# Performance work log

Hardware: AMD Instinct MI355X
Metric: run time of the kernel (lower is better)

## Reference

```python
import jax, jax.numpy as jnp
import numpy as np

ETA = 0.5  # from init_kwargs; eta >= 0 branch
N = 16777216

def setup_inputs() -> dict:
    key = jax.random.key(0)
    k1, k2 = jax.random.split(key)
    outputs = jax.random.normal(k1, (N,), dtype=jnp.float32)
    # PNU targets in {-1, 0, 1}
    targets = jax.random.randint(k2, (N,), 0, 3, dtype=jnp.int32) - 1
    p_ratio = jnp.array([0.4, 0.6], dtype=jnp.float32)
    return {"outputs": outputs, "targets": targets, "p_ratio": p_ratio}

def reference(outputs, targets, p_ratio):
    y = outputs.reshape(-1)
    t = targets.reshape(-1).astype(y.dtype)

    # masks (computed once, fused)
    idx_p = jnp.maximum(t, 0.0)          # positive examples
    idx_n = jnp.maximum(-t, 0.0)         # negative examples
    idx_u = 1.0 - jnp.abs(t)             # unlabeled examples

    sig_neg = jax.nn.sigmoid(-y)         # loss_func(-y)
    sig_pos = jax.nn.sigmoid(y)          # loss_func(-(-y))

    n_p = jnp.maximum(1.0, jnp.sum(idx_p))
    n_n = jnp.maximum(1.0, jnp.sum(idx_n))
    n_u = jnp.maximum(1.0, jnp.sum(idx_u))

    R_P_plus  = jnp.sum(idx_p * sig_neg) / n_p
    R_P_minus = jnp.sum(idx_p * sig_pos) / n_p
    R_N_minus = jnp.sum(idx_n * sig_pos) / n_n
    R_U_minus = jnp.sum(idx_u * sig_pos) / n_u

    R_PN = p_ratio[0] * R_P_plus + p_ratio[1] * R_N_minus
    R_PU = p_ratio[0] * (R_P_plus - R_P_minus) + R_U_minus

    # eta >= 0 branch
    return (1.0 - ETA) * R_PN + ETA * R_PU
```

## Files before the change

kernel.cpp:

```cpp
#include <hip/hip_runtime.h>

#define ETA 0.5f
#define NTHREADS 256
#define UNROLL 4
#define CHUNK (NTHREADS * UNROLL)
#define NCHUNKS 4
#define NACC 5

__device__ __forceinline__ float wave_reduce_sum(float v) {
#pragma unroll
    for (int off = 32; off > 0; off >>= 1)
        v += __shfl_down(v, off, 64);
    return v;
}

__device__ __forceinline__ void pnu_accum(float yy, int tt,
                                          float& sAll, float& sT, float& sA,
                                          float& cT, float& cA) {
    float s = __builtin_amdgcn_rcpf(1.0f + __expf(-yy));
    float tf = (float)tt;
    float ta = fabsf(tf);
    sAll += s;
    sT = fmaf(tf, s, sT);
    sA = fmaf(ta, s, sA);
    cT += tf;
    cA += ta;
}

#define LOAD_CHUNK(YB, TB, c)                                                \
    do {                                                                     \
        const int base_ = (c) * CHUNK + threadIdx.x;                         \
        _Pragma("unroll")                                                    \
        for (int u = 0; u < UNROLL; ++u) YB[u] = y4[base_ + u * NTHREADS];   \
        _Pragma("unroll")                                                    \
        for (int u = 0; u < UNROLL; ++u) TB[u] = t4[base_ + u * NTHREADS];   \
    } while (0)

#define COMPUTE_CHUNK(YB, TB)                                                \
    do {                                                                     \
        _Pragma("unroll")                                                    \
        for (int u = 0; u < UNROLL; ++u) {                                   \
            pnu_accum(YB[u].x, TB[u].x, sAll, sT, sA, cT, cA);               \
            pnu_accum(YB[u].y, TB[u].y, sAll, sT, sA, cT, cA);               \
            pnu_accum(YB[u].z, TB[u].z, sAll, sT, sA, cT, cA);               \
            pnu_accum(YB[u].w, TB[u].w, sAll, sT, sA, cT, cA);               \
        }                                                                    \
    } while (0)

__global__ __launch_bounds__(NTHREADS, 4) void pnu_partial_kernel(
    const float* __restrict__ y, const int* __restrict__ t,
    float* __restrict__ partials, int n, int nblocks, int nfull, int cpb) {
    const int nvec = n >> 2;
    const float4* __restrict__ y4 = reinterpret_cast<const float4*>(y);
    const int4* __restrict__ t4 = reinterpret_cast<const int4*>(t);

    float sAll = 0.f, sT = 0.f, sA = 0.f, cT = 0.f, cA = 0.f;

    {
        int c = blockIdx.x * cpb;
        int end = c + cpb;
        if (end > nfull) end = nfull;
        if (c < end) {
            float4 yvA[UNROLL], yvB[UNROLL];
            int4 tvA[UNROLL], tvB[UNROLL];
            LOAD_CHUNK(yvA, tvA, c);
            while (c + 2 <= end) {
                LOAD_CHUNK(yvB, tvB, c + 1);
                COMPUTE_CHUNK(yvA, tvA);
                if (c + 2 < end) LOAD_CHUNK(yvA, tvA, c + 2);
                COMPUTE_CHUNK(yvB, tvB);
                c += 2;
            }
            if (c < end) COMPUTE_CHUNK(yvA, tvA);
        }
    }

    if (blockIdx.x == gridDim.x - 1) {
        for (int i = nfull * CHUNK + threadIdx.x; i < nvec; i += NTHREADS) {
            float4 yv = y4[i];
            int4 tv = t4[i];
            pnu_accum(yv.x, tv.x, sAll, sT, sA, cT, cA);
            pnu_accum(yv.y, tv.y, sAll, sT, sA, cT, cA);
            pnu_accum(yv.z, tv.z, sAll, sT, sA, cT, cA);
            pnu_accum(yv.w, tv.w, sAll, sT, sA, cT, cA);
        }
        for (int i = (nvec << 2) + threadIdx.x; i < n; i += NTHREADS)
            pnu_accum(y[i], t[i], sAll, sT, sA, cT, cA);
    }

    float vals[NACC] = {sAll, sT, sA, cT, cA};
    __shared__ float red[NTHREADS / 64][NACC];
    const int lane = threadIdx.x & 63;
    const int wave = threadIdx.x >> 6;
#pragma unroll
    for (int k = 0; k < NACC; ++k) {
        float r = wave_reduce_sum(vals[k]);
        if (lane == 0) red[wave][k] = r;
    }
    __syncthreads();
    if (threadIdx.x < NACC) {
        float r = 0.f;
#pragma unroll
        for (int w = 0; w < NTHREADS / 64; ++w) r += red[w][threadIdx.x];
        partials[threadIdx.x * nblocks + blockIdx.x] = r;
    }
}

#define FTHREADS 1024

__global__ __launch_bounds__(FTHREADS) void pnu_final_kernel(
    const float* __restrict__ partials, const float* __restrict__ p_ratio,
    float* __restrict__ out, int nblocks, int n) {
    float acc[NACC] = {0.f, 0.f, 0.f, 0.f, 0.f};
    for (int i = threadIdx.x; i < nblocks; i += FTHREADS) {
#pragma unroll
        for (int k = 0; k < NACC; ++k) acc[k] += partials[k * nblocks + i];
    }
    __shared__ float red[FTHREADS / 64][NACC];
    const int lane = threadIdx.x & 63;
    const int wave = threadIdx.x >> 6;
#pragma unroll
    for (int k = 0; k < NACC; ++k) {
        float r = wave_reduce_sum(acc[k]);
        if (lane == 0) red[wave][k] = r;
    }
    __syncthreads();
    if (threadIdx.x == 0) {
        float tot[NACC];
#pragma unroll
        for (int k = 0; k < NACC; ++k) {
            float r = 0.f;
#pragma unroll
            for (int w = 0; w < FTHREADS / 64; ++w) r += red[w][k];
            tot[k] = r;
        }
        const float sAll = tot[0], sT = tot[1], sA = tot[2];
        const float cT = tot[3], cA = tot[4];

        const float cP = 0.5f * (cA + cT);
        const float cN = 0.5f * (cA - cT);
        const float cU = (float)n - cA;
        const float sPm = 0.5f * (sA + sT);
        const float sNm = 0.5f * (sA - sT);
        const float sUm = sAll - sA;
        const float sPp = cP - sPm;

        const float nP = fmaxf(1.0f, cP);
        const float nN = fmaxf(1.0f, cN);
        const float nU = fmaxf(1.0f, cU);

        const float R_P_plus  = sPp / nP;
        const float R_P_minus = sPm / nP;
        const float R_N_minus = sNm / nN;
        const float R_U_minus = sUm / nU;

        const float pi0 = p_ratio[0], pi1 = p_ratio[1];
        const float R_PN = pi0 * R_P_plus + pi1 * R_N_minus;
        const float R_PU = pi0 * (R_P_plus - R_P_minus) + R_U_minus;

        out[0] = (1.0f - ETA) * R_PN + ETA * R_PU;
    }
}

extern "C" void kernel_launch(void* const* d_in, const int* in_sizes, int n_in,
                              void* d_out, int out_size, void* d_ws, size_t ws_size,
                              hipStream_t stream) {
    const float* y = (const float*)d_in[0];
    const int* t = (const int*)d_in[1];
    const float* p_ratio = (const float*)d_in[2];
    float* out = (float*)d_out;
    float* partials = (float*)d_ws;

    const int n = in_sizes[0];
    const int nvec = n >> 2;
    const int nfull = nvec / CHUNK;
    const bool tail = (nfull * CHUNK * 4) < n;

    int nblocks = (nfull + NCHUNKS - 1) / NCHUNKS;
    if (tail && nblocks < 1) nblocks = 1;
    if (nblocks < 1) nblocks = 1;

    int maxblocks = (int)(ws_size / (NACC * sizeof(float)));
    if (maxblocks < 1) maxblocks = 1;
    if (nblocks > maxblocks) nblocks = maxblocks;

    const int cpb = (nfull + nblocks - 1) / nblocks;

    pnu_partial_kernel<<<nblocks, NTHREADS, 0, stream>>>(y, t, partials, n,
                                                         nblocks, nfull, cpb);
    pnu_final_kernel<<<1, FTHREADS, 0, stream>>>(partials, p_ratio, out, nblocks, n);
}
```

Measured before the change: 29.89 us.

## Fuse final reduction into partial kernel with last-block atomic ticket

Replaces the separate single-block final reduction kernel with a last-block-done pattern. Each block stores its partials atomically, then takes a ticket from a global counter, and the block holding the last ticket reduces all partials and writes the loss. This removes one kernel launch and its launch gap. In exchange it adds a memset of the counter each call and relies on relaxed atomics plus a waitcnt for ordering, which is a memory-ordering risk.

```diff
diff --git a/kernel.cpp b/kernel.cpp
--- a/kernel.cpp
+++ b/kernel.cpp
@@ -6,6 +6,7 @@
 #define CHUNK (NTHREADS * UNROLL)
 #define NCHUNKS 4
 #define NACC 5
+#define WS_PARTIAL_OFF 64
 
 __device__ __forceinline__ float wave_reduce_sum(float v) {
 #pragma unroll
@@ -47,12 +48,15 @@
         }                                                                    \
     } while (0)
 
-__global__ __launch_bounds__(NTHREADS, 4) void pnu_partial_kernel(
+__global__ __launch_bounds__(NTHREADS, 4) void pnu_fused_kernel(
     const float* __restrict__ y, const int* __restrict__ t,
-    float* __restrict__ partials, int n, int nblocks, int nfull, int cpb) {
+    const float* __restrict__ p_ratio, float* __restrict__ out,
+    float* __restrict__ ws, int n, int nblocks, int nfull, int cpb) {
     const int nvec = n >> 2;
     const float4* __restrict__ y4 = reinterpret_cast<const float4*>(y);
     const int4* __restrict__ t4 = reinterpret_cast<const int4*>(t);
+    float* __restrict__ partials = ws + WS_PARTIAL_OFF;
+    unsigned* __restrict__ counter = reinterpret_cast<unsigned*>(ws);
 
     float sAll = 0.f, sT = 0.f, sA = 0.f, cT = 0.f, cA = 0.f;
 
@@ -102,23 +106,27 @@
         float r = 0.f;
 #pragma unroll
         for (int w = 0; w < NTHREADS / 64; ++w) r += red[w][threadIdx.x];
-        partials[threadIdx.x * nblocks + blockIdx.x] = r;
-    }
-}
-
-#define FTHREADS 1024
-
-__global__ __launch_bounds__(FTHREADS) void pnu_final_kernel(
-    const float* __restrict__ partials, const float* __restrict__ p_ratio,
-    float* __restrict__ out, int nblocks, int n) {
+        __hip_atomic_store(&partials[threadIdx.x * nblocks + blockIdx.x], r,
+                           __ATOMIC_RELAXED, __HIP_MEMORY_SCOPE_AGENT);
+    }
+    __shared__ unsigned sTicket;
+    if (threadIdx.x == 0) {
+        asm volatile("s_waitcnt vmcnt(0)" ::: "memory");
+        sTicket = __hip_atomic_fetch_add(counter, 1u, __ATOMIC_RELAXED,
+                                         __HIP_MEMORY_SCOPE_AGENT);
+    }
+    __syncthreads();
+    if (sTicket != (unsigned)(nblocks - 1)) return;
+
     float acc[NACC] = {0.f, 0.f, 0.f, 0.f, 0.f};
-    for (int i = threadIdx.x; i < nblocks; i += FTHREADS) {
-#pragma unroll
-        for (int k = 0; k < NACC; ++k) acc[k] += partials[k * nblocks + i];
-    }
-    __shared__ float red[FTHREADS / 64][NACC];
-    const int lane = threadIdx.x & 63;
-    const int wave = threadIdx.x >> 6;
+    for (int i = threadIdx.x; i < nblocks; i += NTHREADS) {
+#pragma unroll
+        for (int k = 0; k < NACC; ++k)
+            acc[k] += __hip_atomic_load(&partials[k * nblocks + i],
+                                        __ATOMIC_RELAXED,
+                                        __HIP_MEMORY_SCOPE_AGENT);
+    }
+    __syncthreads();
 #pragma unroll
     for (int k = 0; k < NACC; ++k) {
         float r = wave_reduce_sum(acc[k]);
@@ -131,18 +139,18 @@
         for (int k = 0; k < NACC; ++k) {
             float r = 0.f;
 #pragma unroll
-            for (int w = 0; w < FTHREADS / 64; ++w) r += red[w][k];
+            for (int w = 0; w < NTHREADS / 64; ++w) r += red[w][k];
             tot[k] = r;
         }
-        const float sAll = tot[0], sT = tot[1], sA = tot[2];
-        const float cT = tot[3], cA = tot[4];
-
-        const float cP = 0.5f * (cA + cT);
-        const float cN = 0.5f * (cA - cT);
-        const float cU = (float)n - cA;
-        const float sPm = 0.5f * (sA + sT);
-        const float sNm = 0.5f * (sA - sT);
-        const float sUm = sAll - sA;
+        const float sAllT = tot[0], sTT = tot[1], sAT = tot[2];
+        const float cTT = tot[3], cAT = tot[4];
+
+        const float cP = 0.5f * (cAT + cTT);
+        const float cN = 0.5f * (cAT - cTT);
+        const float cU = (float)n - cAT;
+        const float sPm = 0.5f * (sAT + sTT);
+        const float sNm = 0.5f * (sAT - sTT);
+        const float sUm = sAllT - sAT;
         const float sPp = cP - sPm;
 
         const float nP = fmaxf(1.0f, cP);
@@ -169,7 +177,7 @@
     const int* t = (const int*)d_in[1];
     const float* p_ratio = (const float*)d_in[2];
     float* out = (float*)d_out;
-    float* partials = (float*)d_ws;
+    float* ws = (float*)d_ws;
 
     const int n = in_sizes[0];
     const int nvec = n >> 2;
@@ -177,16 +185,18 @@
     const bool tail = (nfull * CHUNK * 4) < n;
 
     int nblocks = (nfull + NCHUNKS - 1) / NCHUNKS;
-    if (tail && nblocks < 1) nblocks = 1;
     if (nblocks < 1) nblocks = 1;
-
-    int maxblocks = (int)(ws_size / (NACC * sizeof(float)));
-    if (maxblocks < 1) maxblocks = 1;
+    (void)tail;
+
+    size_t cap = (ws_size / sizeof(float));
+    cap = cap > WS_PARTIAL_OFF ? (cap - WS_PARTIAL_OFF) / NACC : 1;
+    int maxblocks = (int)(cap < 1 ? 1 : cap);
     if (nblocks > maxblocks) nblocks = maxblocks;
 
     const int cpb = (nfull + nblocks - 1) / nblocks;
 
-    pnu_partial_kernel<<<nblocks, NTHREADS, 0, stream>>>(y, t, partials, n,
-                                                         nblocks, nfull, cpb);
-    pnu_final_kernel<<<1, FTHREADS, 0, stream>>>(partials, p_ratio, out, nblocks, n);
-}
+    hipMemsetAsync(d_ws, 0, WS_PARTIAL_OFF * sizeof(float), stream);
+
+    pnu_fused_kernel<<<nblocks, NTHREADS, 0, stream>>>(y, t, p_ratio, out, ws,
+                                                       n, nblocks, nfull, cpb);
+}
```

Measured after the change: 38.66 us. 29.3% more time.
